# Kernel optimization log

Hardware: AMD Instinct MI355X
Metric: run time of the kernel (lower is better)

Reference implementation:

```python
import jax, jax.numpy as jnp
import numpy as np

OUT_H, OUT_W = 7, 7
SPATIAL_SCALE = 1.0 / 16.0


def setup_inputs() -> dict:
    key = jax.random.key(0)
    k_fm, k_idx, k_x1, k_y1, k_w, k_h = jax.random.split(key, 6)
    B, C, H, W = 4, 256, 64, 64
    N = 256
    feature_map = jax.random.normal(k_fm, (B, C, H, W), dtype=jnp.float32)
    idx = jax.random.randint(k_idx, (N,), 0, B)
    x1 = jax.random.randint(k_x1, (N,), 0, 500)
    y1 = jax.random.randint(k_y1, (N,), 0, 500)
    bw = jax.random.randint(k_w, (N,), 16, 524)
    bh = jax.random.randint(k_h, (N,), 16, 524)
    x2 = jnp.minimum(x1 + bw, 1023)
    y2 = jnp.minimum(y1 + bh, 1023)
    rois = jnp.stack([idx, x1, y1, x2, y2], axis=1).astype(jnp.int32)
    return {"feature_map": feature_map, "rois": rois}


def _roi_pool(feature_map, rois):
    # Faithful to torch: rois.float(); rois[:,1:] *= spatial_scale; rois.int() (trunc)
    coords = (rois[:, 1:].astype(jnp.float32) * SPATIAL_SCALE).astype(jnp.int32)
    idx = rois[:, 0]
    ltx, lty, rbx, rby = coords[:, 0], coords[:, 1], coords[:, 2], coords[:, 3]
    H, W = feature_map.shape[2], feature_map.shape[3]
    h_roi = rby - lty + 1  # inclusive slice [lty : rby+1]
    w_roi = rbx - ltx + 1

    # adaptive_max_pool2d bin boundaries: start = floor(i*L/O), end = ceil((i+1)*L/O)
    oi = jnp.arange(OUT_H, dtype=jnp.int32)
    oj = jnp.arange(OUT_W, dtype=jnp.int32)
    hstart = lty[:, None] + (oi[None, :] * h_roi[:, None]) // OUT_H          # (N, OH)
    hend = lty[:, None] + -((-(oi[None, :] + 1) * h_roi[:, None]) // OUT_H)  # ceil div
    wstart = ltx[:, None] + (oj[None, :] * w_roi[:, None]) // OUT_W          # (N, OW)
    wend = ltx[:, None] + -((-(oj[None, :] + 1) * w_roi[:, None]) // OUT_W)

    hgrid = jnp.arange(H, dtype=jnp.int32)
    wgrid = jnp.arange(W, dtype=jnp.int32)
    # membership masks; comparisons against grid bounds also reproduce slice clamping
    mask_h = (hgrid[None, None, :] >= hstart[:, :, None]) & (hgrid[None, None, :] < hend[:, :, None])  # (N, OH, H)
    mask_w = (wgrid[None, None, :] >= wstart[:, :, None]) & (wgrid[None, None, :] < wend[:, :, None])  # (N, OW, W)

    feat = feature_map[idx]  # (N, C, H, W) gather of per-ROI image features
    neg = jnp.array(-jnp.inf, dtype=feat.dtype)

    # reduce width per output column (OUT_W is a small static constant)
    cols = []
    for j in range(OUT_W):
        m = mask_w[:, j][:, None, None, :]  # (N,1,1,W)
        cols.append(jnp.max(jnp.where(m, feat, neg), axis=3))  # (N, C, H)
    tmp = jnp.stack(cols, axis=-1)  # (N, C, H, OW)

    rows = []
    for i in range(OUT_H):
        m = mask_h[:, i][:, None, :, None]  # (N,1,H,1)
        rows.append(jnp.max(jnp.where(m, tmp, neg), axis=2))  # (N, C, OW)
    return jnp.stack(rows, axis=2)  # (N, C, OH, OW)


def reference(feature_map, rois):
    return _roi_pool(feature_map, rois)
```

## Files before the change

### kernel.cpp

```cpp
#include <hip/hip_runtime.h>

#define NCH   256
#define FH    64
#define FW    64
#define OUT_H 7
#define OUT_W 7
#define WPB   4
#define MAXH  34
#define LDSW  40

__global__ __launch_bounds__(256) void roipool_kernel(
    const float* __restrict__ fm,
    const int*   __restrict__ rois,
    float*       __restrict__ out)
{
    __shared__ __align__(16) float lds[WPB][MAXH][LDSW];

    const int tid  = threadIdx.x;
    const int wv   = tid >> 6;
    const int lane = tid & 63;
    const int task = __builtin_amdgcn_readfirstlane(blockIdx.x * WPB + wv);
    const int n    = task >> 8;
    const int c    = task & 255;

    const int* r = rois + n * 5;
    const int b  = r[0];
    const int x1 = r[1] >> 4;
    const int y1 = r[2] >> 4;
    const int x2 = r[3] >> 4;
    const int y2 = r[4] >> 4;
    const int h_roi = y2 - y1 + 1;
    const int w_roi = x2 - x1 + 1;
    const int qs  = x1 >> 2;
    const int qn  = (x2 >> 2) - qs + 1;
    const int off = x1 & 3;

    const int hq = h_roi / 7, hr = h_roi - hq * 7;
    const int wq = w_roi / 7, wr = w_roi - wq * 7;
    const int hb  = hq + (hr == 0 ? 0 : (hr == 1 ? 1 : 2));
    const int wbn = wq + (wr == 0 ? 0 : (wr == 1 ? 1 : 2));

    const int rg = lane / 10;
    const int rr = (rg == 6) ? 0 : rg;
    const int qq = lane - rg * 10;
    const int passes = (h_roi + 5) / 6;

    const float4* srcq =
        (const float4*)(fm + (((size_t)(b * NCH + c)) << 12) + ((size_t)y1 << 6)) + qs;
    const bool qok = (qq < qn);

    float4 v0, v1, v2, v3, v4, v5;
    int h0, h1, h2, h3, h4, h5;
    if (qok) {
        h0 = rr;
        v0 = srcq[h0 * (FW / 4) + qq];
        if (passes > 1) { h1 = rr + 6;  h1 = (h1 < h_roi) ? h1 : (h_roi - 1); v1 = srcq[h1 * (FW / 4) + qq]; }
        if (passes > 2) { h2 = rr + 12; h2 = (h2 < h_roi) ? h2 : (h_roi - 1); v2 = srcq[h2 * (FW / 4) + qq]; }
        if (passes > 3) { h3 = rr + 18; h3 = (h3 < h_roi) ? h3 : (h_roi - 1); v3 = srcq[h3 * (FW / 4) + qq]; }
        if (passes > 4) { h4 = rr + 24; h4 = (h4 < h_roi) ? h4 : (h_roi - 1); v4 = srcq[h4 * (FW / 4) + qq]; }
        if (passes > 5) { h5 = rr + 30; h5 = (h5 < h_roi) ? h5 : (h_roi - 1); v5 = srcq[h5 * (FW / 4) + qq]; }

        float4* ldsq = (float4*)&lds[wv][0][0];
        ldsq[h0 * (LDSW / 4) + qq] = v0;
        if (passes > 1) ldsq[h1 * (LDSW / 4) + qq] = v1;
        if (passes > 2) ldsq[h2 * (LDSW / 4) + qq] = v2;
        if (passes > 3) ldsq[h3 * (LDSW / 4) + qq] = v3;
        if (passes > 4) ldsq[h4 * (LDSW / 4) + qq] = v4;
        if (passes > 5) ldsq[h5 * (LDSW / 4) + qq] = v5;
    }

    if (lane < OUT_H * OUT_W) {
        const int i = lane / OUT_W;
        const int j = lane - i * OUT_W;

        const int hs  = (i * h_roi) / OUT_H;
        const int he1 = ((i + 1) * h_roi + 6) / OUT_H - 1;
        const int ws  = (j * w_roi) / OUT_W + off;
        const int we1 = ((j + 1) * w_roi + 6) / OUT_W - 1 + off;

        int cb[6];
        #pragma unroll
        for (int bb = 0; bb < 6; ++bb) {
            const int w = ws + bb;
            cb[bb] = (w < we1) ? w : we1;
        }

        const float* tb = &lds[wv][0][0];
        float m = -INFINITY;
        #pragma unroll
        for (int a = 0; a < 6; ++a) {
            if (a < hb) {
                const int hh = (hs + a < he1) ? hs + a : he1;
                const float* rp = tb + hh * LDSW;
                #pragma unroll
                for (int bb = 0; bb < 6; ++bb) {
                    if (bb < wbn)
                        m = fmaxf(m, rp[cb[bb]]);
                }
            }
        }
        out[(size_t)task * (OUT_H * OUT_W) + lane] = m;
    }
}

extern "C" void kernel_launch(void* const* d_in, const int* in_sizes, int n_in,
                              void* d_out, int out_size, void* d_ws, size_t ws_size,
                              hipStream_t stream) {
    const float* fm   = (const float*)d_in[0];
    const int*   rois = (const int*)d_in[1];
    float*       out  = (float*)d_out;

    const int N = in_sizes[1] / 5;
    dim3 grid((N * NCH) / WPB);
    dim3 block(256);
    roipool_kernel<<<grid, block, 0, stream>>>(fm, rois, out);
}
```

Measured before the change: 27.02 us.

## Precompute per-ROI descriptors and per-cell bin tables in a prep kernel

```diff
diff --git a/kernel.cpp b/kernel.cpp
--- a/kernel.cpp
+++ b/kernel.cpp
@@ -1,7 +1,6 @@
 #include <hip/hip_runtime.h>
 
 #define NCH   256
-#define FH    64
 #define FW    64
 #define OUT_H 7
 #define OUT_W 7
@@ -9,12 +8,47 @@
 #define MAXH  34
 #define LDSW  40
 
+__global__ __launch_bounds__(256) void prep_kernel(
+    const int* __restrict__ rois, int* __restrict__ wsI, int nroi)
+{
+    const int n = blockIdx.x * blockDim.x + threadIdx.x;
+    if (n >= nroi) return;
+    const int b  = rois[n * 5 + 0];
+    const int x1 = rois[n * 5 + 1] >> 4;
+    const int y1 = rois[n * 5 + 2] >> 4;
+    const int x2 = rois[n * 5 + 3] >> 4;
+    const int y2 = rois[n * 5 + 4] >> 4;
+    const int h = y2 - y1 + 1, w = x2 - x1 + 1;
+    const int qs = x1 >> 2, qn = (x2 >> 2) - qs + 1, off = x1 & 3;
+    const int hq = h / 7, hr = h - hq * 7;
+    const int hb = hq + (hr == 0 ? 0 : (hr == 1 ? 1 : 2));
+
+    int* d = wsI + n * 8;
+    d[0] = ((b * NCH) << 12) + (y1 << 6) + (qs << 2);
+    d[1] = (h + 5) / 6;
+    d[2] = qn;
+    d[3] = h - 1;
+    d[4] = hb;
+    d[5] = 0; d[6] = 0; d[7] = 0;
+
+    int* ct = wsI + 2048 + n * 64;
+    for (int cell = 0; cell < 49; ++cell) {
+        const int i = cell / 7, j = cell - i * 7;
+        const int hs  = (i * h) / 7;
+        const int he1 = ((i + 1) * h + 6) / 7 - 1;
+        const int wsr = (j * w) / 7;
+        const int wn  = ((j + 1) * w + 6) / 7 - wsr;
+        const int wsl = wsr + off;
+        ct[cell] = hs | (he1 << 8) | (wsl << 16) | (wn << 24);
+    }
+}
+
 __global__ __launch_bounds__(256) void roipool_kernel(
     const float* __restrict__ fm,
-    const int*   __restrict__ rois,
+    const int*   __restrict__ wsI,
     float*       __restrict__ out)
 {
-    __shared__ __align__(16) float lds[WPB][MAXH][LDSW];
+    __shared__ __align__(16) float lds_all[WPB * MAXH * LDSW + 8];
 
     const int tid  = threadIdx.x;
     const int wv   = tid >> 6;
@@ -23,30 +57,17 @@
     const int n    = task >> 8;
     const int c    = task & 255;
 
-    const int* r = rois + n * 5;
-    const int b  = r[0];
-    const int x1 = r[1] >> 4;
-    const int y1 = r[2] >> 4;
-    const int x2 = r[3] >> 4;
-    const int y2 = r[4] >> 4;
-    const int h_roi = y2 - y1 + 1;
-    const int w_roi = x2 - x1 + 1;
-    const int qs  = x1 >> 2;
-    const int qn  = (x2 >> 2) - qs + 1;
-    const int off = x1 & 3;
+    const int* dsc = wsI + n * 8;
+    const int qoff   = dsc[0];
+    const int passes = dsc[1];
+    const int qn     = dsc[2];
+    const int hm1    = dsc[3];
+    const int hb     = dsc[4];
 
-    const int hq = h_roi / 7, hr = h_roi - hq * 7;
-    const int wq = w_roi / 7, wr = w_roi - wq * 7;
-    const int hb  = hq + (hr == 0 ? 0 : (hr == 1 ? 1 : 2));
-    const int wbn = wq + (wr == 0 ? 0 : (wr == 1 ? 1 : 2));
-
-    const int rg = lane / 10;
+    const int rg = (lane * 6554) >> 16;
     const int rr = (rg == 6) ? 0 : rg;
     const int qq = lane - rg * 10;
-    const int passes = (h_roi + 5) / 6;
-
-    const float4* srcq =
-        (const float4*)(fm + (((size_t)(b * NCH + c)) << 12) + ((size_t)y1 << 6)) + qs;
+    const float4* srcq = (const float4*)fm + (qoff >> 2) + (c << 10);
     const bool qok = (qq < qn);
 
     float4 v0, v1, v2, v3, v4, v5;
@@ -54,13 +75,13 @@
     if (qok) {
         h0 = rr;
         v0 = srcq[h0 * (FW / 4) + qq];
-        if (passes > 1) { h1 = rr + 6;  h1 = (h1 < h_roi) ? h1 : (h_roi - 1); v1 = srcq[h1 * (FW / 4) + qq]; }
-        if (passes > 2) { h2 = rr + 12; h2 = (h2 < h_roi) ? h2 : (h_roi - 1); v2 = srcq[h2 * (FW / 4) + qq]; }
-        if (passes > 3) { h3 = rr + 18; h3 = (h3 < h_roi) ? h3 : (h_roi - 1); v3 = srcq[h3 * (FW / 4) + qq]; }
-        if (passes > 4) { h4 = rr + 24; h4 = (h4 < h_roi) ? h4 : (h_roi - 1); v4 = srcq[h4 * (FW / 4) + qq]; }
-        if (passes > 5) { h5 = rr + 30; h5 = (h5 < h_roi) ? h5 : (h_roi - 1); v5 = srcq[h5 * (FW / 4) + qq]; }
+        if (passes > 1) { h1 = rr + 6;  h1 = (h1 < hm1) ? h1 : hm1; v1 = srcq[h1 * (FW / 4) + qq]; }
+        if (passes > 2) { h2 = rr + 12; h2 = (h2 < hm1) ? h2 : hm1; v2 = srcq[h2 * (FW / 4) + qq]; }
+        if (passes > 3) { h3 = rr + 18; h3 = (h3 < hm1) ? h3 : hm1; v3 = srcq[h3 * (FW / 4) + qq]; }
+        if (passes > 4) { h4 = rr + 24; h4 = (h4 < hm1) ? h4 : hm1; v4 = srcq[h4 * (FW / 4) + qq]; }
+        if (passes > 5) { h5 = rr + 30; h5 = (h5 < hm1) ? h5 : hm1; v5 = srcq[h5 * (FW / 4) + qq]; }
 
-        float4* ldsq = (float4*)&lds[wv][0][0];
+        float4* ldsq = (float4*)(lds_all + wv * (MAXH * LDSW));
         ldsq[h0 * (LDSW / 4) + qq] = v0;
         if (passes > 1) ldsq[h1 * (LDSW / 4) + qq] = v1;
         if (passes > 2) ldsq[h2 * (LDSW / 4) + qq] = v2;
@@ -70,33 +91,27 @@
     }
 
     if (lane < OUT_H * OUT_W) {
-        const int i = lane / OUT_W;
-        const int j = lane - i * OUT_W;
+        const int cd  = (wsI + 2048 + n * 64)[lane];
+        const int hs  = cd & 0xff;
+        const int he1 = (cd >> 8) & 0xff;
+        const int wsl = (cd >> 16) & 0xff;
+        const int wn  = cd >> 24;
 
-        const int hs  = (i * h_roi) / OUT_H;
-        const int he1 = ((i + 1) * h_roi + 6) / OUT_H - 1;
-        const int ws  = (j * w_roi) / OUT_W + off;
-        const int we1 = ((j + 1) * w_roi + 6) / OUT_W - 1 + off;
-
-        int cb[6];
-        #pragma unroll
-        for (int bb = 0; bb < 6; ++bb) {
-            const int w = ws + bb;
-            cb[bb] = (w < we1) ? w : we1;
-        }
-
-        const float* tb = &lds[wv][0][0];
+        const float* tb = lds_all + wv * (MAXH * LDSW);
         float m = -INFINITY;
         #pragma unroll
         for (int a = 0; a < 6; ++a) {
             if (a < hb) {
                 const int hh = (hs + a < he1) ? hs + a : he1;
-                const float* rp = tb + hh * LDSW;
-                #pragma unroll
-                for (int bb = 0; bb < 6; ++bb) {
-                    if (bb < wbn)
-                        m = fmaxf(m, rp[cb[bb]]);
-                }
+                const float* rp = tb + hh * LDSW + wsl;
+                const float r0 = rp[0], r1 = rp[1], r2 = rp[2];
+                const float r3 = rp[3], r4 = rp[4], r5 = rp[5];
+                m = fmaxf(m, r0);
+                m = fmaxf(m, (1 < wn) ? r1 : -INFINITY);
+                m = fmaxf(m, (2 < wn) ? r2 : -INFINITY);
+                m = fmaxf(m, (3 < wn) ? r3 : -INFINITY);
+                m = fmaxf(m, (4 < wn) ? r4 : -INFINITY);
+                m = fmaxf(m, (5 < wn) ? r5 : -INFINITY);
             }
         }
         out[(size_t)task * (OUT_H * OUT_W) + lane] = m;
@@ -109,9 +124,11 @@
     const float* fm   = (const float*)d_in[0];
     const int*   rois = (const int*)d_in[1];
     float*       out  = (float*)d_out;
+    int*         wsI  = (int*)d_ws;
 
     const int N = in_sizes[1] / 5;
+    prep_kernel<<<dim3((N + 255) / 256), 256, 0, stream>>>(rois, wsI, N);
+
     dim3 grid((N * NCH) / WPB);
-    dim3 block(256);
-    roipool_kernel<<<grid, block, 0, stream>>>(fm, rois, out);
+    roipool_kernel<<<grid, dim3(256), 0, stream>>>(fm, wsI, out);
 }
```

Result: slower. 32.43 us (+20.0%).
